# Kernel tuning notes

Hardware: AMD Instinct MI355X
Metric: run time of the kernel (lower is better)

## Reference

```python
import jax, jax.numpy as jnp
import numpy as np

# DCT-III (a.k.a. IDCT), unnormalized, scaled to match the DREAMPlace kernel:
#   y_k = x_0 + 2 * sum_{n=1}^{N-1} x_n * cos(pi * n * (2k+1) / (2N))
# (the docstring's Re{1/2 x0 + sum xn e^{j pi n (2k+1)/(2N)}} scaled by 2).
# Computed in O(N log N) via a length-2N FFT:
#   y_k = Re{ sum_n c_n x_n e^{j pi n/(2N)} e^{2 pi j n k/(2N)} }
# which is 2N * ifft(pad(a, 2N)) evaluated at k = 0..N-1, with
#   a_n = c_n * x_n * exp(j pi n / (2N)),  c_0 = 1, c_{n>0} = 2.

def _idct_last_dim(x):
    N = x.shape[-1]
    n = jnp.arange(N)
    c = jnp.where(n == 0, 1.0, 2.0).astype(x.dtype)
    twiddle = jnp.exp(1j * (jnp.pi / (2 * N)) * n.astype(jnp.float32)).astype(jnp.complex64)
    a = (c * x).astype(jnp.complex64) * twiddle          # [.., N]
    y = jnp.fft.ifft(a, n=2 * N, axis=-1)                # [.., 2N]
    return (y.real[..., :N] * (2 * N)).astype(x.dtype)


def setup_inputs() -> dict:
    key = jax.random.key(0)
    x = jax.random.normal(key, (4096, 4096), dtype=jnp.float32)
    return {"x": x}


def reference(x) -> jnp.ndarray:
    return _idct_last_dim(x)
```

## Files before the change

### kernel.cpp

```cpp
#include <hip/hip_runtime.h>
#include <cstdint>


#define NN 4096
#define HH 2048
#define BM 128
#define BN 128
#define BK 64
#define NT (HH / BK)

typedef int i32x4 __attribute__((ext_vector_type(4)));
typedef int i32x2 __attribute__((ext_vector_type(2)));

__device__ __forceinline__ void async_copy16(void* lds_base, const void* gptr) {
    __builtin_amdgcn_global_load_lds(
        (const __attribute__((address_space(1))) unsigned int*)gptr,
        (__attribute__((address_space(3))) unsigned int*)lds_base,
        16, 0, 0);
}

__device__ __forceinline__ int pack4(int q0, int q1, int q2, int q3) {
    return (q0 & 255) | ((q1 & 255) << 8) | ((q2 & 255) << 16) | ((q3 & 255) << 24);
}

__global__ __launch_bounds__(256) void prep_i8(const float* __restrict__ x,
                                               signed char* __restrict__ Ae,
                                               signed char* __restrict__ Ao,
                                               signed char* __restrict__ CEm,
                                               signed char* __restrict__ COm,
                                               float* __restrict__ se,
                                               float* __restrict__ so) {
    const int b = blockIdx.x;
    const int t = threadIdx.x;
    const float s = 3.834951969714103e-4f;

    if (b < 4096) {
        __shared__ float wmaxe[4], wmaxo[4];
        const float* xr = x + (size_t)b * NN;
        float v[16];
#pragma unroll
        for (int j = 0; j < 4; ++j) {
            float4 f = ((const float4*)xr)[t * 4 + j];
            v[j * 4 + 0] = f.x; v[j * 4 + 1] = f.y;
            v[j * 4 + 2] = f.z; v[j * 4 + 3] = f.w;
        }
        float emax = 1e-30f, omax = 1e-30f;
#pragma unroll
        for (int i = 0; i < 8; ++i) {
            emax = fmaxf(emax, __builtin_fabsf(v[2 * i]));
            omax = fmaxf(omax, __builtin_fabsf(v[2 * i + 1]));
        }
#pragma unroll
        for (int m = 1; m < 64; m <<= 1) {
            emax = fmaxf(emax, __shfl_xor(emax, m));
            omax = fmaxf(omax, __shfl_xor(omax, m));
        }
        const int wv = t >> 6;
        if ((t & 63) == 0) { wmaxe[wv] = emax; wmaxo[wv] = omax; }
        __syncthreads();
        const float rmax_e = fmaxf(fmaxf(wmaxe[0], wmaxe[1]), fmaxf(wmaxe[2], wmaxe[3]));
        const float rmax_o = fmaxf(fmaxf(wmaxo[0], wmaxo[1]), fmaxf(wmaxo[2], wmaxo[3]));
        const float inv_e = 127.0f / rmax_e, inv_o = 127.0f / rmax_o;
        int qe[8], qo[8];
#pragma unroll
        for (int i = 0; i < 8; ++i) {
            qe[i] = (int)rintf(v[2 * i] * inv_e);
            qo[i] = (int)rintf(v[2 * i + 1] * inv_o);
        }
        i32x2 oe, oo;
        oe[0] = pack4(qe[0], qe[1], qe[2], qe[3]);
        oe[1] = pack4(qe[4], qe[5], qe[6], qe[7]);
        oo[0] = pack4(qo[0], qo[1], qo[2], qo[3]);
        oo[1] = pack4(qo[4], qo[5], qo[6], qo[7]);
        ((i32x2*)(Ae + (size_t)b * HH))[t] = oe;
        ((i32x2*)(Ao + (size_t)b * HH))[t] = oo;
        if (t == 0) {
            se[b] = rmax_e * (1.0f / 127.0f);
            so[b] = rmax_o * (1.0f / 127.0f);
        }
    } else if (b < 6144) {
        const int k = b - 4096;
        const int twok1 = 2 * k + 1;
        int q[8];
#pragma unroll
        for (int i = 0; i < 8; ++i) {
            int m = t * 8 + i;
            int p = (2 * m * twok1) & 16383;
            float w = (m == 0) ? 1.0f : 2.0f;
            q[i] = (int)rintf(w * __cosf((float)p * s) * 63.5f);
        }
        i32x2 o;
        o[0] = pack4(q[0], q[1], q[2], q[3]);
        o[1] = pack4(q[4], q[5], q[6], q[7]);
        ((i32x2*)(CEm + (size_t)k * HH))[t] = o;
    } else {
        const int k = b - 6144;
        const int twok1 = 2 * k + 1;
        int q[8];
#pragma unroll
        for (int i = 0; i < 8; ++i) {
            int m = t * 8 + i;
            int p = ((2 * m + 1) * twok1) & 16383;
            q[i] = (int)rintf(__cosf((float)p * s) * 127.0f);
        }
        i32x2 o;
        o[0] = pack4(q[0], q[1], q[2], q[3]);
        o[1] = pack4(q[4], q[5], q[6], q[7]);
        ((i32x2*)(COm + (size_t)k * HH))[t] = o;
    }
}

__global__ __launch_bounds__(256, 2) void idct_gemm2(const signed char* __restrict__ Ae,
                                                     const signed char* __restrict__ Ao,
                                                     const signed char* __restrict__ CEm,
                                                     const signed char* __restrict__ COm,
                                                     const float* __restrict__ se,
                                                     const float* __restrict__ so,
                                                     float* __restrict__ C) {
    __shared__ __align__(16) signed char sAe[2][BM * BK];
    __shared__ __align__(16) signed char sAo[2][BM * BK];
    __shared__ __align__(16) signed char sCE[2][BN * BK];
    __shared__ __align__(16) signed char sCO[2][BN * BK];

    const int tid  = threadIdx.x;
    const int wave = tid >> 6;
    const int lane = tid & 63;
    const int waveM = wave >> 1;
    const int waveN = wave & 1;

    const int rowBase = blockIdx.y * BM;
    const int colBase = blockIdx.x * BN;

    i32x4 accE[4][4] = {};
    i32x4 accO[4][4] = {};

    const int srow  = lane >> 2;
    const int sgran = lane & 3;
    const int ggcol = (sgran ^ ((srow >> 1) & 3)) * 16;
    const int quad  = lane >> 4;
    const int fsw   = (lane >> 1) & 3;
    const int poff  = (quad ^ fsw) * 16;
    const int ck0   = wave * 2;

    const size_t aRow = (size_t)(rowBase + ck0 * 16 + srow) * HH + ggcol;
    const size_t bRow = (size_t)(colBase + ck0 * 16 + srow) * HH + ggcol;

#define STAGE(BUF, K0)                                                        \
    do {                                                                      \
        _Pragma("unroll")                                                     \
        for (int j = 0; j < 2; ++j) {                                         \
            size_t aoff = aRow + (size_t)j * 16 * HH + (size_t)(K0);          \
            size_t boff = bRow + (size_t)j * 16 * HH + (size_t)(K0);          \
            async_copy16(&sAe[BUF][(ck0 + j) * 1024], Ae + aoff);             \
            async_copy16(&sAo[BUF][(ck0 + j) * 1024], Ao + aoff);             \
            async_copy16(&sCE[BUF][(ck0 + j) * 1024], CEm + boff);            \
            async_copy16(&sCO[BUF][(ck0 + j) * 1024], COm + boff);            \
        }                                                                     \
    } while (0)

#define COMPUTE(BUF)                                                          \
    do {                                                                      \
        i32x4 af[4], bfr[4];                                                  \
        _Pragma("unroll")                                                     \
        for (int mi = 0; mi < 4; ++mi)                                        \
            af[mi] = *(const i32x4*)&sAe[BUF][(waveM * 64 + mi * 16 + (lane & 15)) * BK + poff]; \
        _Pragma("unroll")                                                     \
        for (int ni = 0; ni < 4; ++ni)                                        \
            bfr[ni] = *(const i32x4*)&sCE[BUF][(waveN * 64 + ni * 16 + (lane & 15)) * BK + poff]; \
        __builtin_amdgcn_s_setprio(1);                                        \
        _Pragma("unroll")                                                     \
        for (int mi = 0; mi < 4; ++mi)                                        \
            _Pragma("unroll")                                                 \
            for (int ni = 0; ni < 4; ++ni)                                    \
                accE[mi][ni] = __builtin_amdgcn_mfma_i32_16x16x64_i8(         \
                    af[mi], bfr[ni], accE[mi][ni], 0, 0, 0);                  \
        __builtin_amdgcn_s_setprio(0);                                        \
        _Pragma("unroll")                                                     \
        for (int mi = 0; mi < 4; ++mi)                                        \
            af[mi] = *(const i32x4*)&sAo[BUF][(waveM * 64 + mi * 16 + (lane & 15)) * BK + poff]; \
        _Pragma("unroll")                                                     \
        for (int ni = 0; ni < 4; ++ni)                                        \
            bfr[ni] = *(const i32x4*)&sCO[BUF][(waveN * 64 + ni * 16 + (lane & 15)) * BK + poff]; \
        __builtin_amdgcn_s_setprio(1);                                        \
        _Pragma("unroll")                                                     \
        for (int mi = 0; mi < 4; ++mi)                                        \
            _Pragma("unroll")                                                 \
            for (int ni = 0; ni < 4; ++ni)                                    \
                accO[mi][ni] = __builtin_amdgcn_mfma_i32_16x16x64_i8(         \
                    af[mi], bfr[ni], accO[mi][ni], 0, 0, 0);                  \
        __builtin_amdgcn_s_setprio(0);                                        \
    } while (0)

    STAGE(0, 0);

#pragma unroll 1
    for (int t = 0; t < NT - 2; t += 2) {
        STAGE(1, (t + 1) * BK);
        asm volatile("s_waitcnt vmcnt(8)" ::: "memory");
        __builtin_amdgcn_s_barrier();
        COMPUTE(0);
        __builtin_amdgcn_s_barrier();

        STAGE(0, (t + 2) * BK);
        asm volatile("s_waitcnt vmcnt(8)" ::: "memory");
        __builtin_amdgcn_s_barrier();
        COMPUTE(1);
        __builtin_amdgcn_s_barrier();
    }
    STAGE(1, (NT - 1) * BK);
    asm volatile("s_waitcnt vmcnt(8)" ::: "memory");
    __builtin_amdgcn_s_barrier();
    COMPUTE(0);
    __builtin_amdgcn_s_barrier();

    asm volatile("s_waitcnt vmcnt(0)" ::: "memory");
    __builtin_amdgcn_s_barrier();
    COMPUTE(1);
#undef STAGE
#undef COMPUTE

    const float sB_s = 2.0f / 127.0f;
    const int mrow0 = rowBase + waveM * 64 + (lane >> 4) * 4;
    const int ncol0 = colBase + waveN * 64 + (lane & 15);
#pragma unroll
    for (int mi = 0; mi < 4; ++mi)
#pragma unroll
        for (int ni = 0; ni < 4; ++ni)
#pragma unroll
            for (int rg = 0; rg < 4; ++rg) {
                int rr = mrow0 + mi * 16 + rg;
                int cc = ncol0 + ni * 16;
                float e = (float)accE[mi][ni][rg] * (se[rr] * sB_s);
                float o = (float)accO[mi][ni][rg] * (so[rr] * sB_s);
                C[(size_t)rr * NN + cc] = e + o;
                C[(size_t)rr * NN + (NN - 1 - cc)] = e - o;
            }
}

__global__ __launch_bounds__(256) void idct_naive(const float* __restrict__ x,
                                                  float* __restrict__ out) {
    int row = blockIdx.x;
    __shared__ float sx[NN];
    for (int i = threadIdx.x; i < NN; i += 256) sx[i] = x[(size_t)row * NN + i];
    __syncthreads();
    const float s = 3.834951969714103e-4f;
    for (int k = threadIdx.x; k < NN; k += 256) {
        int twok1 = 2 * k + 1;
        float acc = sx[0];
        int p = 0;
        for (int n = 1; n < NN; ++n) {
            p += twok1; p &= 16383;
            acc += 2.0f * sx[n] * __cosf((float)p * s);
        }
        out[(size_t)row * NN + k] = acc;
    }
}

extern "C" void kernel_launch(void* const* d_in, const int* in_sizes, int n_in,
                              void* d_out, int out_size, void* d_ws, size_t ws_size,
                              hipStream_t stream) {
    const float* x = (const float*)d_in[0];
    float* out = (float*)d_out;

    const size_t eA = (size_t)NN * HH;
    const size_t eC = (size_t)HH * HH;
    const size_t need = 2 * eA + 2 * eC + 2 * NN * sizeof(float);

    if (ws_size >= need) {
        signed char* Ae = (signed char*)d_ws;
        signed char* Ao = Ae + eA;
        signed char* CEm = Ao + eA;
        signed char* COm = CEm + eC;
        float* se = (float*)(COm + eC);
        float* so = se + NN;

        prep_i8<<<8192, 256, 0, stream>>>(x, Ae, Ao, CEm, COm, se, so);

        dim3 grid(HH / BN, NN / BM);
        idct_gemm2<<<grid, 256, 0, stream>>>(Ae, Ao, CEm, COm, se, so, out);
    } else {
        idct_naive<<<NN, 256, 0, stream>>>(x, out);
    }
}
```

Baseline: 153.6 us.

## Use BK=128 single-buffered tiles with split even/odd staging and grouped block order

The K tile grows from 64 to 128, and the double buffer is replaced by one buffer per operand. The even and odd GEMM halves are staged alternately, so one half's load overlaps the other half's MFMA compute. The LDS swizzle is changed to an 8-granule XOR to fit the wider rows. Blocks are also remapped into 8x8 groups to improve L2 reuse of A and cosine rows. This cuts barrier count per K and may improve cache locality, but it exposes load latency when the alternating overlap is insufficient. It also drops the s_setprio hints.

```diff
diff --git a/kernel.cpp b/kernel.cpp
--- a/kernel.cpp
+++ b/kernel.cpp
@@ -6,8 +6,7 @@
 #define HH 2048
 #define BM 128
 #define BN 128
-#define BK 64
-#define NT (HH / BK)
+#define BK 128
 
 typedef int i32x4 __attribute__((ext_vector_type(4)));
 typedef int i32x2 __attribute__((ext_vector_type(2)));
@@ -117,10 +116,10 @@
                                                      const float* __restrict__ se,
                                                      const float* __restrict__ so,
                                                      float* __restrict__ C) {
-    __shared__ __align__(16) signed char sAe[2][BM * BK];
-    __shared__ __align__(16) signed char sAo[2][BM * BK];
-    __shared__ __align__(16) signed char sCE[2][BN * BK];
-    __shared__ __align__(16) signed char sCO[2][BN * BK];
+    __shared__ __align__(16) signed char sAe[BM * BK];
+    __shared__ __align__(16) signed char sAo[BM * BK];
+    __shared__ __align__(16) signed char sCE[BN * BK];
+    __shared__ __align__(16) signed char sCO[BN * BK];
 
     const int tid  = threadIdx.x;
     const int wave = tid >> 6;
@@ -128,96 +127,106 @@
     const int waveM = wave >> 1;
     const int waveN = wave & 1;
 
-    const int rowBase = blockIdx.y * BM;
-    const int colBase = blockIdx.x * BN;
+    const int lid = blockIdx.y * gridDim.x + blockIdx.x;
+    const int q8  = lid & 7;
+    const int jj  = lid >> 3;
+    const int bx  = (q8 & 1) * 8 + (jj & 7);
+    const int by  = (q8 >> 1) * 8 + (jj >> 3);
+
+    const int rowBase = by * BM;
+    const int colBase = bx * BN;
 
     i32x4 accE[4][4] = {};
     i32x4 accO[4][4] = {};
 
-    const int srow  = lane >> 2;
-    const int sgran = lane & 3;
-    const int ggcol = (sgran ^ ((srow >> 1) & 3)) * 16;
+    const int srow  = lane >> 3;
+    const int sgran = lane & 7;
+    const int ggcol = (sgran ^ srow) * 16;
+    const int rmod  = lane & 7;
     const int quad  = lane >> 4;
-    const int fsw   = (lane >> 1) & 3;
-    const int poff  = (quad ^ fsw) * 16;
-    const int ck0   = wave * 2;
-
-    const size_t aRow = (size_t)(rowBase + ck0 * 16 + srow) * HH + ggcol;
-    const size_t bRow = (size_t)(colBase + ck0 * 16 + srow) * HH + ggcol;
-
-#define STAGE(BUF, K0)                                                        \
+
+#define STAGE_E(K0)                                                           \
     do {                                                                      \
         _Pragma("unroll")                                                     \
-        for (int j = 0; j < 2; ++j) {                                         \
-            size_t aoff = aRow + (size_t)j * 16 * HH + (size_t)(K0);          \
-            size_t boff = bRow + (size_t)j * 16 * HH + (size_t)(K0);          \
-            async_copy16(&sAe[BUF][(ck0 + j) * 1024], Ae + aoff);             \
-            async_copy16(&sAo[BUF][(ck0 + j) * 1024], Ao + aoff);             \
-            async_copy16(&sCE[BUF][(ck0 + j) * 1024], CEm + boff);            \
-            async_copy16(&sCO[BUF][(ck0 + j) * 1024], COm + boff);            \
+        for (int j = 0; j < 4; ++j) {                                         \
+            int ck = wave * 4 + j;                                            \
+            int r  = ck * 8 + srow;                                           \
+            size_t aoff = (size_t)(rowBase + r) * HH + (K0) + ggcol;          \
+            size_t boff = (size_t)(colBase + r) * HH + (K0) + ggcol;          \
+            async_copy16(&sAe[ck * 1024], Ae + aoff);                         \
+            async_copy16(&sCE[ck * 1024], CEm + boff);                        \
         }                                                                     \
     } while (0)
 
-#define COMPUTE(BUF)                                                          \
+#define STAGE_O(K0)                                                           \
     do {                                                                      \
-        i32x4 af[4], bfr[4];                                                  \
         _Pragma("unroll")                                                     \
-        for (int mi = 0; mi < 4; ++mi)                                        \
-            af[mi] = *(const i32x4*)&sAe[BUF][(waveM * 64 + mi * 16 + (lane & 15)) * BK + poff]; \
+        for (int j = 0; j < 4; ++j) {                                         \
+            int ck = wave * 4 + j;                                            \
+            int r  = ck * 8 + srow;                                           \
+            size_t aoff = (size_t)(rowBase + r) * HH + (K0) + ggcol;          \
+            size_t boff = (size_t)(colBase + r) * HH + (K0) + ggcol;          \
+            async_copy16(&sAo[ck * 1024], Ao + aoff);                         \
+            async_copy16(&sCO[ck * 1024], COm + boff);                        \
+        }                                                                     \
+    } while (0)
+
+#define COMPUTE_PAIR(SA, SC, ACC)                                             \
+    do {                                                                      \
         _Pragma("unroll")                                                     \
-        for (int ni = 0; ni < 4; ++ni)                                        \
-            bfr[ni] = *(const i32x4*)&sCE[BUF][(waveN * 64 + ni * 16 + (lane & 15)) * BK + poff]; \
-        __builtin_amdgcn_s_setprio(1);                                        \
-        _Pragma("unroll")                                                     \
-        for (int mi = 0; mi < 4; ++mi)                                        \
+        for (int kk = 0; kk < 2; ++kk) {                                      \
+            const int poff = ((kk * 4 + quad) ^ rmod) * 16;                   \
+            i32x4 af[4], bfr[4];                                              \
             _Pragma("unroll")                                                 \
-            for (int ni = 0; ni < 4; ++ni)                                    \
-                accE[mi][ni] = __builtin_amdgcn_mfma_i32_16x16x64_i8(         \
-                    af[mi], bfr[ni], accE[mi][ni], 0, 0, 0);                  \
-        __builtin_amdgcn_s_setprio(0);                                        \
-        _Pragma("unroll")                                                     \
-        for (int mi = 0; mi < 4; ++mi)                                        \
-            af[mi] = *(const i32x4*)&sAo[BUF][(waveM * 64 + mi * 16 + (lane & 15)) * BK + poff]; \
-        _Pragma("unroll")                                                     \
-        for (int ni = 0; ni < 4; ++ni)                                        \
-            bfr[ni] = *(const i32x4*)&sCO[BUF][(waveN * 64 + ni * 16 + (lane & 15)) * BK + poff]; \
-        __builtin_amdgcn_s_setprio(1);                                        \
-        _Pragma("unroll")                                                     \
-        for (int mi = 0; mi < 4; ++mi)                                        \
+            for (int mi = 0; mi < 4; ++mi) {                                  \
+                int r = waveM * 64 + mi * 16 + (lane & 15);                   \
+                af[mi] = *(const i32x4*)&SA[r * BK + poff];                   \
+            }                                                                 \
             _Pragma("unroll")                                                 \
-            for (int ni = 0; ni < 4; ++ni)                                    \
-                accO[mi][ni] = __builtin_amdgcn_mfma_i32_16x16x64_i8(         \
-                    af[mi], bfr[ni], accO[mi][ni], 0, 0, 0);                  \
-        __builtin_amdgcn_s_setprio(0);                                        \
+            for (int ni = 0; ni < 4; ++ni) {                                  \
+                int r = waveN * 64 + ni * 16 + (lane & 15);                   \
+                bfr[ni] = *(const i32x4*)&SC[r * BK + poff];                  \
+            }                                                                 \
+            _Pragma("unroll")                                                 \
+            for (int mi = 0; mi < 4; ++mi)                                    \
+                _Pragma("unroll")                                             \
+                for (int ni = 0; ni < 4; ++ni)                                \
+                    ACC[mi][ni] = __builtin_amdgcn_mfma_i32_16x16x64_i8(      \
+                        af[mi], bfr[ni], ACC[mi][ni], 0, 0, 0);               \
+        }                                                                     \
     } while (0)
 
-    STAGE(0, 0);
+    STAGE_E(0);
+    STAGE_O(0);
 
 #pragma unroll 1
-    for (int t = 0; t < NT - 2; t += 2) {
-        STAGE(1, (t + 1) * BK);
+    for (int t = 0; t < 15; ++t) {
         asm volatile("s_waitcnt vmcnt(8)" ::: "memory");
         __builtin_amdgcn_s_barrier();
-        COMPUTE(0);
-        __builtin_amdgcn_s_barrier();
-
-        STAGE(0, (t + 2) * BK);
+        asm volatile("" ::: "memory");
+        COMPUTE_PAIR(sAe, sCE, accE);
+        __builtin_amdgcn_s_barrier();
+        STAGE_E((t + 1) * BK);
+
         asm volatile("s_waitcnt vmcnt(8)" ::: "memory");
         __builtin_amdgcn_s_barrier();
-        COMPUTE(1);
-        __builtin_amdgcn_s_barrier();
-    }
-    STAGE(1, (NT - 1) * BK);
+        asm volatile("" ::: "memory");
+        COMPUTE_PAIR(sAo, sCO, accO);
+        __builtin_amdgcn_s_barrier();
+        STAGE_O((t + 1) * BK);
+    }
     asm volatile("s_waitcnt vmcnt(8)" ::: "memory");
     __builtin_amdgcn_s_barrier();
-    COMPUTE(0);
+    asm volatile("" ::: "memory");
+    COMPUTE_PAIR(sAe, sCE, accE);
     __builtin_amdgcn_s_barrier();
-
     asm volatile("s_waitcnt vmcnt(0)" ::: "memory");
     __builtin_amdgcn_s_barrier();
-    COMPUTE(1);
-#undef STAGE
-#undef COMPUTE
+    asm volatile("" ::: "memory");
+    COMPUTE_PAIR(sAo, sCO, accO);
+#undef STAGE_E
+#undef STAGE_O
+#undef COMPUTE_PAIR
 
     const float sB_s = 2.0f / 127.0f;
     const int mrow0 = rowBase + waveM * 64 + (lane >> 4) * 4;
```

Result: faster. 146.1 us (-4.9%).
